# Performance work log

Measured on AMD Instinct MI355X. Metric: run time of the kernel, lower is better.

Reference implementation:

```python
import jax, jax.numpy as jnp
import numpy as np

B, S, H = 2, 2048, 1024
E, K, F = 8, 2, 4096


def setup_inputs() -> dict:
    key = jax.random.key(0)
    ks = jax.random.split(key, 7)
    s_h = 1.0 / np.sqrt(H)
    s_f = 1.0 / np.sqrt(F)
    return {
        "hidden_states": jax.random.normal(ks[0], (B, S, H), jnp.float32),
        "Wr": jax.random.normal(ks[1], (H, E), jnp.float32) * s_h,
        "br": jnp.zeros((E,), jnp.float32),
        "W1": jax.random.normal(ks[2], (E, H, F), jnp.float32) * s_h,
        "b1": jnp.zeros((E, F), jnp.float32),
        "W2": jax.random.normal(ks[3], (E, F, H), jnp.float32) * s_f,
        "b2": jnp.zeros((E, H), jnp.float32),
    }


def _moe_forward(hidden_states, Wr, br, W1, b1, W2, b2):
    b, s, h = hidden_states.shape
    x = hidden_states.reshape(-1, h)  # [T, H]
    # --- router: top-k over softmax probs, renormalized ---
    logits = x @ Wr + br  # [T, E]
    probs = jax.nn.softmax(logits, axis=-1)
    top_w, top_i = jax.lax.top_k(probs, K)  # [T, K]
    weights = top_w / jnp.sum(top_w, axis=-1, keepdims=True)  # [T, K]
    # --- dense-equivalent expert dispatch + combine ---
    # per-token per-expert combine weight (zero for unselected experts)
    out = jnp.zeros_like(x)
    for e in range(E):
        w_e = jnp.sum(weights * (top_i == e), axis=-1)  # [T]
        h_e = jax.nn.gelu(x @ W1[e] + b1[e], approximate=False)  # [T, F]
        y_e = h_e @ W2[e] + b2[e]  # [T, H]
        out = out + w_e[:, None] * y_e
    # --- aux load-balance loss (counts are constants wrt grads) ---
    counts = jnp.sum(jax.nn.one_hot(top_i, E, dtype=logits.dtype), axis=(0, 1))  # [E]
    load = counts / (top_i.size)
    aux_loss = jnp.mean((load - 1.0 / E) ** 2)
    # --- z-loss ---
    z_loss = jnp.mean(jax.nn.logsumexp(logits, axis=-1))
    total_loss = 0.01 * aux_loss + 0.001 * z_loss
    return out.reshape(b, s, h), total_loss


def reference(hidden_states, Wr, br, W1, b1, W2, b2):
    output, total_loss = _moe_forward(hidden_states, Wr, br, W1, b1, W2, b2)
    return output, total_loss
```

## Files before the change

kernel.cpp:

```cpp
#include <hip/hip_runtime.h>
#include <stdint.h>
#include <math.h>

#define T_TOK 4096
#define H_DIM 1024
#define E_EXP 8
#define F_DIM 4096
#define NASSIGN (T_TOK * 2)
#define OUT_ELEMS ((size_t)T_TOK * H_DIM)
#define YB_ELEMS ((size_t)8192 * H_DIM)
#define TL 257

typedef unsigned short u16;
typedef __attribute__((ext_vector_type(8))) short short8;
typedef __attribute__((ext_vector_type(4))) short short4v;
typedef __attribute__((ext_vector_type(4))) float f32x4;

__device__ __forceinline__ u16 f2bf(float f) {
  union { float f; uint32_t u; } c; c.f = f;
  uint32_t u = c.u;
  return (u16)((u + 0x7FFFu + ((u >> 16) & 1u)) >> 16);
}

__device__ __forceinline__ float fast_erf(float u) {
  const float au = fabsf(u);
  const float t = __builtin_amdgcn_rcpf(__builtin_fmaf(0.3275911f, au, 1.0f));
  float p = __builtin_fmaf(1.061405429f, t, -1.453152027f);
  p = __builtin_fmaf(p, t, 1.421413741f);
  p = __builtin_fmaf(p, t, -0.284496736f);
  p = __builtin_fmaf(p, t, 0.254829592f);
  p = p * t;
  const float y = __builtin_fmaf(-p, __expf(-au * au), 1.0f);
  return copysignf(y, u);
}

__device__ __forceinline__ void gl_lds16(const void* g, void* l) {
  __builtin_amdgcn_global_load_lds(
      (const __attribute__((address_space(1))) uint32_t*)g,
      (__attribute__((address_space(3))) uint32_t*)(uintptr_t)l, 16, 0, 0);
}

__device__ __forceinline__ void transpose_strip(
    const float* __restrict__ in, u16* __restrict__ out, int R, int C,
    int bx , int by , int bz, u16* tile) {
  const size_t eoff = (size_t)bz * R * C;
  const int wave = threadIdx.x >> 6, lane = threadIdx.x & 63;
  const float* inp = in + eoff + ((size_t)by * 64) * C + bx * 256;
#pragma unroll
  for (int p = 0; p < 16; ++p) {
    const int r = p * 4 + wave;
    const float4 v = *(const float4*)(inp + (size_t)r * C + lane * 4);
    u16* trow = tile + r * TL + lane * 4;
    trow[0] = f2bf(v.x); trow[1] = f2bf(v.y); trow[2] = f2bf(v.z); trow[3] = f2bf(v.w);
  }
  __syncthreads();
  const int cl = threadIdx.x >> 3;
  const int rg = (threadIdx.x & 7) * 8;
#pragma unroll
  for (int tx = 0; tx < 4; ++tx) {
    u16* op = out + (((size_t)bz * (C >> 6) + bx * 4 + tx) * (R >> 6) + by) * 4096;
#pragma unroll
    for (int p = 0; p < 2; ++p) {
      const int c = cl + p * 32;
      short8 o;
#pragma unroll
      for (int j = 0; j < 8; ++j) o[j] = (short)tile[(rg + j) * TL + tx * 64 + c];
      *(short8*)(op + c * 64 + rg) = o;
    }
  }
}

__global__ __launch_bounds__(256) void prep_kernel(
    const float* __restrict__ x, const float* __restrict__ Wr,
    const float* __restrict__ br, u16* __restrict__ xb,
    int* __restrict__ tki, float* __restrict__ tkw,
    int* __restrict__ counts, float* __restrict__ zsum,
    const float* __restrict__ W1, u16* __restrict__ w1t,
    const float* __restrict__ W2, u16* __restrict__ w2t) {
  __shared__ u16 tile[64 * TL];
  __shared__ int lcnt[8];
  __shared__ float lzv[16];
  const int id = blockIdx.x;

  if (id >= 256) {
    if (id < 2304) {
      const int q = id - 256;
      transpose_strip(W1, w1t, H_DIM, F_DIM, q & 15, (q >> 4) & 15, q >> 8, tile);
    } else {
      const int q = id - 2304;
      transpose_strip(W2, w2t, F_DIM, H_DIM, q & 3, (q >> 2) & 63, q >> 8, tile);
    }
    return;
  }

  const int wave = threadIdx.x >> 6;
  const int lane = threadIdx.x & 63;
  if (threadIdx.x < 8) lcnt[threadIdx.x] = 0;
  __syncthreads();
#pragma unroll
  for (int it = 0; it < 4; ++it) {
    const int t = id * 16 + wave * 4 + it;
    const float* xr = x + (size_t)t * H_DIM;
    u16* xbr = xb + (size_t)t * H_DIM;
    float acc[8];
#pragma unroll
    for (int e = 0; e < 8; ++e) acc[e] = 0.0f;
#pragma unroll
    for (int j = 0; j < 4; ++j) {
      const int h0 = j * 256 + lane * 4;
      const float4 xv = *(const float4*)(xr + h0);
      const float vv[4] = {xv.x, xv.y, xv.z, xv.w};
      short4v pk;
#pragma unroll
      for (int i = 0; i < 4; ++i) {
        pk[i] = (short)f2bf(vv[i]);
        const float4 w0 = *(const float4*)(Wr + (size_t)(h0 + i) * 8);
        const float4 w1 = *(const float4*)(Wr + (size_t)(h0 + i) * 8 + 4);
        acc[0] += vv[i] * w0.x; acc[1] += vv[i] * w0.y;
        acc[2] += vv[i] * w0.z; acc[3] += vv[i] * w0.w;
        acc[4] += vv[i] * w1.x; acc[5] += vv[i] * w1.y;
        acc[6] += vv[i] * w1.z; acc[7] += vv[i] * w1.w;
      }
      *(short4v*)(xbr + h0) = pk;
    }
#pragma unroll
    for (int e = 0; e < 8; ++e) {
      float v = acc[e];
#pragma unroll
      for (int s = 32; s > 0; s >>= 1) v += __shfl_xor(v, s);
      acc[e] = v;
    }
    if (lane == 0) {
      float l[8];
#pragma unroll
      for (int e = 0; e < 8; ++e) l[e] = acc[e] + br[e];
      float mx = l[0];
#pragma unroll
      for (int e = 1; e < 8; ++e) mx = fmaxf(mx, l[e]);
      float p[8], s = 0.0f;
#pragma unroll
      for (int e = 0; e < 8; ++e) { p[e] = __expf(l[e] - mx); s += p[e]; }
      int i0 = 0;
#pragma unroll
      for (int e = 1; e < 8; ++e) if (p[e] > p[i0]) i0 = e;
      int i1 = (i0 == 0) ? 1 : 0;
#pragma unroll
      for (int e = 0; e < 8; ++e) if (e != i1 && e != i0 && p[e] > p[i1]) i1 = e;
      const float ws = p[i0] + p[i1];
      tki[2 * t] = i0; tki[2 * t + 1] = i1;
      tkw[2 * t] = p[i0] / ws; tkw[2 * t + 1] = p[i1] / ws;
      atomicAdd(&lcnt[i0], 1);
      atomicAdd(&lcnt[i1], 1);
      lzv[wave * 4 + it] = mx + logf(s);
    }
  }
  __syncthreads();
  if (threadIdx.x < 8) {
    const int c = lcnt[threadIdx.x];
    if (c) atomicAdd(&counts[threadIdx.x], c);
  }
  if (threadIdx.x == 64) {
    float zs = 0.0f;
#pragma unroll
    for (int i = 0; i < 16; ++i) zs += lzv[i];
    atomicAdd(zsum, zs);
  }
}

__global__ void scatter_kernel(const int* __restrict__ tki, const float* __restrict__ tkw,
                               const int* __restrict__ counts, int* __restrict__ cursor,
                               int* __restrict__ perm, float* __restrict__ pw,
                               int* __restrict__ islot,
                               const float* __restrict__ zsum, float* __restrict__ out_loss) {
  int offs[8];
  {
    int a = 0;
#pragma unroll
    for (int e = 0; e < 8; ++e) { offs[e] = a; a += counts[e]; }
  }
  const int lane = threadIdx.x & 63;
  const int t = blockIdx.x * 256 + threadIdx.x;
#pragma unroll
  for (int k = 0; k < 2; ++k) {
    const int e = tki[2 * t + k];
    int slot = 0;
#pragma unroll
    for (int ee = 0; ee < 8; ++ee) {
      const unsigned long long mask = __ballot(e == ee);
      if (mask) {
        const int leader = __ffsll(mask) - 1;
        int b = 0;
        if (lane == leader) b = atomicAdd(&cursor[ee], (int)__popcll(mask));
        b = __shfl(b, leader);
        if (e == ee) {
          const int r = (int)__popcll(mask & ((1ull << lane) - 1ull));
          slot = offs[ee] + b + r;
        }
      }
    }
    perm[slot] = t;
    pw[slot] = tkw[2 * t + k];
    islot[2 * t + k] = slot;
  }
  if (blockIdx.x == 0 && threadIdx.x == 0) {
    float aux = 0.0f;
#pragma unroll
    for (int e = 0; e < 8; ++e) {
      const float d = (float)counts[e] / (float)NASSIGN - 0.125f;
      aux += d * d;
    }
    aux *= (1.0f / 8.0f);
    out_loss[0] = 0.01f * aux + 0.001f * (zsum[0] / (float)T_TOK);
  }
}


__global__ __launch_bounds__(256, 4) void gemm1_kernel(
    const u16* __restrict__ xb, const u16* __restrict__ w1t,
    const float* __restrict__ b1, const int* __restrict__ perm,
    const int* __restrict__ cnts, u16* __restrict__ hbuf) {
  const int id = blockIdx.x;
  const int e = id & 7;
  const int wq = id >> 3;
  const int n0 = (wq & 31) << 7;
  const int m0 = (wq >> 5) << 7;
  int cnt, off;
  {
    int a = 0, c = 0;
#pragma unroll
    for (int i = 0; i < 8; ++i) { const int ci = cnts[i]; if (i < e) a += ci; if (i == e) c = ci; }
    cnt = c; off = a;
  }
  if (m0 >= cnt) return;

  __shared__ __align__(16) u16 smem[16384];
  u16* As = smem;
  u16* Bs = smem + 8192;

  const int tid = threadIdx.x;
  const int rbase = tid >> 3;
  const int kc = ((tid & 7) ^ (rbase & 7)) * 8;

  const u16* ap[4];
#pragma unroll
  for (int l = 0; l < 4; ++l) {
    int ra = m0 + rbase + l * 32; if (ra > cnt - 1) ra = cnt - 1;
    ap[l] = xb + (size_t)perm[off + ra] * H_DIM + kc;
  }
  const u16* bp0 = w1t + ((((size_t)e * (F_DIM >> 6) + (n0 >> 6)) * (H_DIM >> 6)) << 12)
                 + rbase * 64 + kc;
  const size_t bnt = (size_t)(H_DIM >> 6) << 12;

  const int wave = tid >> 6, lane = tid & 63;
  const int wm = (wave >> 1) * 64, wn = (wave & 1) * 64;
  const int lr = lane & 15, q = lane >> 4;
  const int qs0 = q ^ (lr & 7), qs1 = (4 + q) ^ (lr & 7);

  f32x4 acc[4][4];
#pragma unroll
  for (int i = 0; i < 4; ++i)
#pragma unroll
    for (int j = 0; j < 4; ++j) acc[i][j] = (f32x4)0.0f;

  const short8* Afr = (const short8*)As;
  const short8* Bfr = (const short8*)Bs;

  for (int k0 = 0; k0 < (H_DIM >> 6); ++k0) {
    gl_lds16(ap[0], &As[(size_t)tid * 8]);
    gl_lds16(ap[1], &As[(size_t)(tid + 256) * 8]);
    gl_lds16(ap[2], &As[(size_t)(tid + 512) * 8]);
    gl_lds16(ap[3], &As[(size_t)(tid + 768) * 8]);
    gl_lds16(bp0,              &Bs[(size_t)tid * 8]);
    gl_lds16(bp0 + 2048,       &Bs[(size_t)(tid + 256) * 8]);
    gl_lds16(bp0 + bnt,        &Bs[(size_t)(tid + 512) * 8]);
    gl_lds16(bp0 + bnt + 2048, &Bs[(size_t)(tid + 768) * 8]);
#pragma unroll
    for (int l = 0; l < 4; ++l) ap[l] += 64;
    bp0 += 4096;
    __syncthreads();
#pragma unroll
    for (int s = 0; s < 2; ++s) {
      const int qs = s ? qs1 : qs0;
      short8 a[4], b[4];
#pragma unroll
      for (int i = 0; i < 4; ++i) a[i] = Afr[(wm + i * 16 + lr) * 8 + qs];
#pragma unroll
      for (int j = 0; j < 4; ++j) b[j] = Bfr[(wn + j * 16 + lr) * 8 + qs];
#pragma unroll
      for (int i = 0; i < 4; ++i)
#pragma unroll
        for (int j = 0; j < 4; ++j)
          acc[i][j] = __builtin_amdgcn_mfma_f32_16x16x32_bf16(a[i], b[j], acc[i][j], 0, 0, 0);
    }
    __syncthreads();
  }

#pragma unroll
  for (int i = 0; i < 4; ++i) {
#pragma unroll
    for (int rr = 0; rr < 4; ++rr) {
      const int row = wm + i * 16 + q * 4 + rr;
#pragma unroll
      for (int j = 0; j < 4; ++j) {
        const int col = wn + j * 16 + lr;
        const float v = acc[i][j][rr] + b1[e * F_DIM + n0 + col];
        const float g = 0.5f * v * (1.0f + fast_erf(v * 0.70710678118654752f));
        smem[(row << 7) + (col ^ (q << 4))] = f2bf(g);
      }
    }
  }
  __syncthreads();
#pragma unroll
  for (int p = 0; p < 8; ++p) {
    const int ml = p * 16 + (tid >> 4);
    const int nl = (tid & 15) * 8;
    const int m = m0 + ml;
    if (m < cnt) {
      const int qq = (ml >> 2) & 3;
      *(short8*)(hbuf + (size_t)(off + m) * F_DIM + n0 + nl) =
          *(const short8*)(smem + (ml << 7) + (nl ^ (qq << 4)));
    }
  }
}

__global__ __launch_bounds__(256, 4) void gemm2_kernel(
    const u16* __restrict__ hbuf, const u16* __restrict__ w2t,
    const float* __restrict__ b2, const float* __restrict__ pw,
    const int* __restrict__ cnts, float* __restrict__ ybuf) {
  const int id = blockIdx.x;
  const int e = id & 7;
  const int wq = id >> 3;
  const int n0 = (wq & 7) << 7;
  const int ks = (wq >> 3) & 1;
  const int m0 = (wq >> 4) << 7;
  int cnt, off;
  {
    int a = 0, c = 0;
#pragma unroll
    for (int i = 0; i < 8; ++i) { const int ci = cnts[i]; if (i < e) a += ci; if (i == e) c = ci; }
    cnt = c; off = a;
  }
  if (m0 >= cnt) return;

  __shared__ __align__(16) u16 As[128 * 64];
  __shared__ __align__(16) u16 Bs[128 * 64];

  const int tid = threadIdx.x;
  const int rbase = tid >> 3;
  const int kc = ((tid & 7) ^ (rbase & 7)) * 8;

  const u16* ap[4];
#pragma unroll
  for (int l = 0; l < 4; ++l) {
    int ra = m0 + rbase + l * 32; if (ra > cnt - 1) ra = cnt - 1;
    ap[l] = hbuf + (size_t)(off + ra) * F_DIM + (ks << 11) + kc;
  }
  const u16* bp0 = w2t + ((((size_t)e * (H_DIM >> 6) + (n0 >> 6)) * (F_DIM >> 6)) << 12)
                 + ((size_t)(ks << 5) << 12) + rbase * 64 + kc;
  const size_t bnt = (size_t)(F_DIM >> 6) << 12;

  const int wave = tid >> 6, lane = tid & 63;
  const int wm = (wave >> 1) * 64, wn = (wave & 1) * 64;
  const int lr = lane & 15, q = lane >> 4;
  const int qs0 = q ^ (lr & 7), qs1 = (4 + q) ^ (lr & 7);

  f32x4 acc[4][4];
#pragma unroll
  for (int i = 0; i < 4; ++i)
#pragma unroll
    for (int j = 0; j < 4; ++j) acc[i][j] = (f32x4)0.0f;

  const short8* Afr = (const short8*)As;
  const short8* Bfr = (const short8*)Bs;

  for (int k0 = 0; k0 < 32; ++k0) {
    gl_lds16(ap[0], &As[(size_t)tid * 8]);
    gl_lds16(ap[1], &As[(size_t)(tid + 256) * 8]);
    gl_lds16(ap[2], &As[(size_t)(tid + 512) * 8]);
    gl_lds16(ap[3], &As[(size_t)(tid + 768) * 8]);
    gl_lds16(bp0,              &Bs[(size_t)tid * 8]);
    gl_lds16(bp0 + 2048,       &Bs[(size_t)(tid + 256) * 8]);
    gl_lds16(bp0 + bnt,        &Bs[(size_t)(tid + 512) * 8]);
    gl_lds16(bp0 + bnt + 2048, &Bs[(size_t)(tid + 768) * 8]);
#pragma unroll
    for (int l = 0; l < 4; ++l) ap[l] += 64;
    bp0 += 4096;
    __syncthreads();
#pragma unroll
    for (int s = 0; s < 2; ++s) {
      const int qs = s ? qs1 : qs0;
      short8 a[4], b[4];
#pragma unroll
      for (int i = 0; i < 4; ++i) a[i] = Afr[(wm + i * 16 + lr) * 8 + qs];
#pragma unroll
      for (int j = 0; j < 4; ++j) b[j] = Bfr[(wn + j * 16 + lr) * 8 + qs];
#pragma unroll
      for (int i = 0; i < 4; ++i)
#pragma unroll
        for (int j = 0; j < 4; ++j)
          acc[i][j] = __builtin_amdgcn_mfma_f32_16x16x32_bf16(a[i], b[j], acc[i][j], 0, 0, 0);
    }
    __syncthreads();
  }

  float* yb = ybuf + (size_t)ks * YB_ELEMS;
#pragma unroll
  for (int i = 0; i < 4; ++i) {
#pragma unroll
    for (int rr = 0; rr < 4; ++rr) {
      const int m = m0 + wm + i * 16 + q * 4 + rr;
      if (m < cnt) {
        const int slot = off + m;
        const float w = pw[slot];
        float* orow = yb + (size_t)slot * H_DIM;
#pragma unroll
        for (int j = 0; j < 4; ++j) {
          const int col = n0 + wn + j * 16 + lr;
          float y = acc[i][j][rr];
          if (ks == 0) y += b2[e * H_DIM + col];
          orow[col] = w * y;
        }
      }
    }
  }
}

__global__ __launch_bounds__(256) void combine_kernel(
    const float* __restrict__ ybuf, const int* __restrict__ islot,
    float* __restrict__ out) {
  const int t = blockIdx.x;
  const int s0 = islot[2 * t];
  const int s1 = islot[2 * t + 1];
  const int c = threadIdx.x * 4;
  const float4 a0 = *(const float4*)(ybuf + (size_t)s0 * H_DIM + c);
  const float4 a1 = *(const float4*)(ybuf + YB_ELEMS + (size_t)s0 * H_DIM + c);
  const float4 b0 = *(const float4*)(ybuf + (size_t)s1 * H_DIM + c);
  const float4 b1 = *(const float4*)(ybuf + YB_ELEMS + (size_t)s1 * H_DIM + c);
  float4 r;
  r.x = a0.x + a1.x + b0.x + b1.x;
  r.y = a0.y + a1.y + b0.y + b1.y;
  r.z = a0.z + a1.z + b0.z + b1.z;
  r.w = a0.w + a1.w + b0.w + b1.w;
  *(float4*)(out + (size_t)t * H_DIM + c) = r;
}


extern "C" void kernel_launch(void* const* d_in, const int* in_sizes, int n_in,
                              void* d_out, int out_size, void* d_ws, size_t ws_size,
                              hipStream_t stream) {
  const float* x  = (const float*)d_in[0];
  const float* Wr = (const float*)d_in[1];
  const float* br = (const float*)d_in[2];
  const float* W1 = (const float*)d_in[3];
  const float* b1 = (const float*)d_in[4];
  const float* W2 = (const float*)d_in[5];
  const float* b2 = (const float*)d_in[6];
  float* out = (float*)d_out;

  char* ws = (char*)d_ws;
  u16* xb    = (u16*)(ws);
  u16* w1t   = (u16*)(ws + 8388608ull);
  u16* w2t   = (u16*)(ws + 75497472ull);
  u16* hbuf  = (u16*)(ws + 142606336ull);
  float* ybuf = (float*)(ws + 8388608ull);
  int*   tki    = (int*)(ws + 209715200ull);
  float* tkw    = (float*)(ws + 209747968ull);
  int*   perm   = (int*)(ws + 209780736ull);
  float* pw     = (float*)(ws + 209813504ull);
  int*   counts = (int*)(ws + 209846272ull);
  int*   cursor = counts + 8;
  float* zsum   = (float*)(counts + 16);
  int*   islot  = (int*)(ws + 209846400ull);

  hipMemsetAsync(counts, 0, 128, stream);

  prep_kernel<<<4352, 256, 0, stream>>>(x, Wr, br, xb, tki, tkw, counts, zsum,
                                        W1, w1t, W2, w2t);
  scatter_kernel<<<T_TOK / 256, 256, 0, stream>>>(tki, tkw, counts, cursor, perm, pw,
                                                  islot, zsum, out + OUT_ELEMS);
  gemm1_kernel<<<8192, 256, 0, stream>>>(xb, w1t, b1, perm, counts, hbuf);
  gemm2_kernel<<<4096, 256, 0, stream>>>(hbuf, w2t, b2, pw, counts, ybuf);
  combine_kernel<<<T_TOK, 256, 0, stream>>>(ybuf, islot, out);
}
```

Measured before the change: 605.9 us.

## Enlarge expert GEMM M-tile to 256 rows per block with 128x64 warp tiles

Both grouped expert GEMMs now process 256 token rows per block instead of 128, with each wave computing a 128x64 sub-tile (8x4 MFMA accumulators). This doubles reuse of each loaded weight tile and halves B-matrix global traffic per output. The GEMM1 epilogue is split into two halves so the existing shared staging buffer can still be reused. In exchange, register pressure and LDS per block rise (occupancy hint lowered to 2), and padding waste grows for experts whose token count is not a multiple of 256.

```diff
diff --git a/kernel.cpp b/kernel.cpp
--- a/kernel.cpp
+++ b/kernel.cpp
@@ -215,7 +215,7 @@
 }
 
 
-__global__ __launch_bounds__(256, 4) void gemm1_kernel(
+__global__ __launch_bounds__(256, 2) void gemm1_kernel(
     const u16* __restrict__ xb, const u16* __restrict__ w1t,
     const float* __restrict__ b1, const int* __restrict__ perm,
     const int* __restrict__ cnts, u16* __restrict__ hbuf) {
@@ -223,7 +223,7 @@
   const int e = id & 7;
   const int wq = id >> 3;
   const int n0 = (wq & 31) << 7;
-  const int m0 = (wq >> 5) << 7;
+  const int m0 = (wq >> 5) << 8;
   int cnt, off;
   {
     int a = 0, c = 0;
@@ -233,17 +233,17 @@
   }
   if (m0 >= cnt) return;
 
-  __shared__ __align__(16) u16 smem[16384];
+  __shared__ __align__(16) u16 smem[24576];
   u16* As = smem;
-  u16* Bs = smem + 8192;
+  u16* Bs = smem + 16384;
 
   const int tid = threadIdx.x;
   const int rbase = tid >> 3;
   const int kc = ((tid & 7) ^ (rbase & 7)) * 8;
 
-  const u16* ap[4];
-#pragma unroll
-  for (int l = 0; l < 4; ++l) {
+  const u16* ap[8];
+#pragma unroll
+  for (int l = 0; l < 8; ++l) {
     int ra = m0 + rbase + l * 32; if (ra > cnt - 1) ra = cnt - 1;
     ap[l] = xb + (size_t)perm[off + ra] * H_DIM + kc;
   }
@@ -252,13 +252,13 @@
   const size_t bnt = (size_t)(H_DIM >> 6) << 12;
 
   const int wave = tid >> 6, lane = tid & 63;
-  const int wm = (wave >> 1) * 64, wn = (wave & 1) * 64;
+  const int wm = (wave >> 1) * 128, wn = (wave & 1) * 64;
   const int lr = lane & 15, q = lane >> 4;
   const int qs0 = q ^ (lr & 7), qs1 = (4 + q) ^ (lr & 7);
 
-  f32x4 acc[4][4];
-#pragma unroll
-  for (int i = 0; i < 4; ++i)
+  f32x4 acc[8][4];
+#pragma unroll
+  for (int i = 0; i < 8; ++i)
 #pragma unroll
     for (int j = 0; j < 4; ++j) acc[i][j] = (f32x4)0.0f;
 
@@ -266,28 +266,27 @@
   const short8* Bfr = (const short8*)Bs;
 
   for (int k0 = 0; k0 < (H_DIM >> 6); ++k0) {
-    gl_lds16(ap[0], &As[(size_t)tid * 8]);
-    gl_lds16(ap[1], &As[(size_t)(tid + 256) * 8]);
-    gl_lds16(ap[2], &As[(size_t)(tid + 512) * 8]);
-    gl_lds16(ap[3], &As[(size_t)(tid + 768) * 8]);
+#pragma unroll
+    for (int l = 0; l < 8; ++l) {
+      gl_lds16(ap[l], &As[(size_t)(tid + l * 256) * 8]);
+      ap[l] += 64;
+    }
     gl_lds16(bp0,              &Bs[(size_t)tid * 8]);
     gl_lds16(bp0 + 2048,       &Bs[(size_t)(tid + 256) * 8]);
     gl_lds16(bp0 + bnt,        &Bs[(size_t)(tid + 512) * 8]);
     gl_lds16(bp0 + bnt + 2048, &Bs[(size_t)(tid + 768) * 8]);
-#pragma unroll
-    for (int l = 0; l < 4; ++l) ap[l] += 64;
     bp0 += 4096;
     __syncthreads();
 #pragma unroll
     for (int s = 0; s < 2; ++s) {
       const int qs = s ? qs1 : qs0;
-      short8 a[4], b[4];
-#pragma unroll
-      for (int i = 0; i < 4; ++i) a[i] = Afr[(wm + i * 16 + lr) * 8 + qs];
+      short8 a[8], b[4];
+#pragma unroll
+      for (int i = 0; i < 8; ++i) a[i] = Afr[(wm + i * 16 + lr) * 8 + qs];
 #pragma unroll
       for (int j = 0; j < 4; ++j) b[j] = Bfr[(wn + j * 16 + lr) * 8 + qs];
 #pragma unroll
-      for (int i = 0; i < 4; ++i)
+      for (int i = 0; i < 8; ++i)
 #pragma unroll
         for (int j = 0; j < 4; ++j)
           acc[i][j] = __builtin_amdgcn_mfma_f32_16x16x32_bf16(a[i], b[j], acc[i][j], 0, 0, 0);
@@ -296,34 +295,40 @@
   }
 
 #pragma unroll
-  for (int i = 0; i < 4; ++i) {
-#pragma unroll
-    for (int rr = 0; rr < 4; ++rr) {
-      const int row = wm + i * 16 + q * 4 + rr;
-#pragma unroll
-      for (int j = 0; j < 4; ++j) {
-        const int col = wn + j * 16 + lr;
-        const float v = acc[i][j][rr] + b1[e * F_DIM + n0 + col];
-        const float g = 0.5f * v * (1.0f + fast_erf(v * 0.70710678118654752f));
-        smem[(row << 7) + (col ^ (q << 4))] = f2bf(g);
+  for (int h = 0; h < 2; ++h) {
+    if ((wave >> 1) == h) {
+#pragma unroll
+      for (int i = 0; i < 8; ++i) {
+#pragma unroll
+        for (int rr = 0; rr < 4; ++rr) {
+          const int rloc = i * 16 + q * 4 + rr;
+#pragma unroll
+          for (int j = 0; j < 4; ++j) {
+            const int col = wn + j * 16 + lr;
+            const float v = acc[i][j][rr] + b1[e * F_DIM + n0 + col];
+            const float g = 0.5f * v * (1.0f + fast_erf(v * 0.70710678118654752f));
+            smem[(rloc << 7) + (col ^ (q << 4))] = f2bf(g);
+          }
+        }
       }
     }
-  }
-  __syncthreads();
-#pragma unroll
-  for (int p = 0; p < 8; ++p) {
-    const int ml = p * 16 + (tid >> 4);
-    const int nl = (tid & 15) * 8;
-    const int m = m0 + ml;
-    if (m < cnt) {
-      const int qq = (ml >> 2) & 3;
-      *(short8*)(hbuf + (size_t)(off + m) * F_DIM + n0 + nl) =
-          *(const short8*)(smem + (ml << 7) + (nl ^ (qq << 4)));
-    }
-  }
-}
-
-__global__ __launch_bounds__(256, 4) void gemm2_kernel(
+    __syncthreads();
+#pragma unroll
+    for (int p = 0; p < 8; ++p) {
+      const int ml = p * 16 + (tid >> 4);
+      const int nl = (tid & 15) * 8;
+      const int m = m0 + h * 128 + ml;
+      if (m < cnt) {
+        const int qq = (ml >> 2) & 3;
+        *(short8*)(hbuf + (size_t)(off + m) * F_DIM + n0 + nl) =
+            *(const short8*)(smem + (ml << 7) + (nl ^ (qq << 4)));
+      }
+    }
+    __syncthreads();
+  }
+}
+
+__global__ __launch_bounds__(256, 2) void gemm2_kernel(
     const u16* __restrict__ hbuf, const u16* __restrict__ w2t,
     const float* __restrict__ b2, const float* __restrict__ pw,
     const int* __restrict__ cnts, float* __restrict__ ybuf) {
@@ -332,7 +337,7 @@
   const int wq = id >> 3;
   const int n0 = (wq & 7) << 7;
   const int ks = (wq >> 3) & 1;
-  const int m0 = (wq >> 4) << 7;
+  const int m0 = (wq >> 4) << 8;
   int cnt, off;
   {
     int a = 0, c = 0;
@@ -342,16 +347,17 @@
   }
   if (m0 >= cnt) return;
 
-  __shared__ __align__(16) u16 As[128 * 64];
-  __shared__ __align__(16) u16 Bs[128 * 64];
+  __shared__ __align__(16) u16 smem[24576];
+  u16* As = smem;
+  u16* Bs = smem + 16384;
 
   const int tid = threadIdx.x;
   const int rbase = tid >> 3;
   const int kc = ((tid & 7) ^ (rbase & 7)) * 8;
 
-  const u16* ap[4];
-#pragma unroll
-  for (int l = 0; l < 4; ++l) {
+  const u16* ap[8];
+#pragma unroll
+  for (int l = 0; l < 8; ++l) {
     int ra = m0 + rbase + l * 32; if (ra > cnt - 1) ra = cnt - 1;
     ap[l] = hbuf + (size_t)(off + ra) * F_DIM + (ks << 11) + kc;
   }
@@ -360,13 +366,13 @@
   const size_t bnt = (size_t)(F_DIM >> 6) << 12;
 
   const int wave = tid >> 6, lane = tid & 63;
-  const int wm = (wave >> 1) * 64, wn = (wave & 1) * 64;
+  const int wm = (wave >> 1) * 128, wn = (wave & 1) * 64;
   const int lr = lane & 15, q = lane >> 4;
   const int qs0 = q ^ (lr & 7), qs1 = (4 + q) ^ (lr & 7);
 
-  f32x4 acc[4][4];
-#pragma unroll
-  for (int i = 0; i < 4; ++i)
+  f32x4 acc[8][4];
+#pragma unroll
+  for (int i = 0; i < 8; ++i)
 #pragma unroll
     for (int j = 0; j < 4; ++j) acc[i][j] = (f32x4)0.0f;
 
@@ -374,28 +380,27 @@
   const short8* Bfr = (const short8*)Bs;
 
   for (int k0 = 0; k0 < 32; ++k0) {
-    gl_lds16(ap[0], &As[(size_t)tid * 8]);
-    gl_lds16(ap[1], &As[(size_t)(tid + 256) * 8]);
-    gl_lds16(ap[2], &As[(size_t)(tid + 512) * 8]);
-    gl_lds16(ap[3], &As[(size_t)(tid + 768) * 8]);
+#pragma unroll
+    for (int l = 0; l < 8; ++l) {
+      gl_lds16(ap[l], &As[(size_t)(tid + l * 256) * 8]);
+      ap[l] += 64;
+    }
     gl_lds16(bp0,              &Bs[(size_t)tid * 8]);
     gl_lds16(bp0 + 2048,       &Bs[(size_t)(tid + 256) * 8]);
     gl_lds16(bp0 + bnt,        &Bs[(size_t)(tid + 512) * 8]);
     gl_lds16(bp0 + bnt + 2048, &Bs[(size_t)(tid + 768) * 8]);
-#pragma unroll
-    for (int l = 0; l < 4; ++l) ap[l] += 64;
     bp0 += 4096;
     __syncthreads();
 #pragma unroll
     for (int s = 0; s < 2; ++s) {
       const int qs = s ? qs1 : qs0;
-      short8 a[4], b[4];
-#pragma unroll
-      for (int i = 0; i < 4; ++i) a[i] = Afr[(wm + i * 16 + lr) * 8 + qs];
+      short8 a[8], b[4];
+#pragma unroll
+      for (int i = 0; i < 8; ++i) a[i] = Afr[(wm + i * 16 + lr) * 8 + qs];
 #pragma unroll
       for (int j = 0; j < 4; ++j) b[j] = Bfr[(wn + j * 16 + lr) * 8 + qs];
 #pragma unroll
-      for (int i = 0; i < 4; ++i)
+      for (int i = 0; i < 8; ++i)
 #pragma unroll
         for (int j = 0; j < 4; ++j)
           acc[i][j] = __builtin_amdgcn_mfma_f32_16x16x32_bf16(a[i], b[j], acc[i][j], 0, 0, 0);
@@ -405,7 +410,7 @@
 
   float* yb = ybuf + (size_t)ks * YB_ELEMS;
 #pragma unroll
-  for (int i = 0; i < 4; ++i) {
+  for (int i = 0; i < 8; ++i) {
 #pragma unroll
     for (int rr = 0; rr < 4; ++rr) {
       const int m = m0 + wm + i * 16 + q * 4 + rr;
@@ -478,7 +483,7 @@
                                         W1, w1t, W2, w2t);
   scatter_kernel<<<T_TOK / 256, 256, 0, stream>>>(tki, tkw, counts, cursor, perm, pw,
                                                   islot, zsum, out + OUT_ELEMS);
-  gemm1_kernel<<<8192, 256, 0, stream>>>(xb, w1t, b1, perm, counts, hbuf);
-  gemm2_kernel<<<4096, 256, 0, stream>>>(hbuf, w2t, b2, pw, counts, ybuf);
+  gemm1_kernel<<<4096, 256, 0, stream>>>(xb, w1t, b1, perm, counts, hbuf);
+  gemm2_kernel<<<2048, 256, 0, stream>>>(hbuf, w2t, b2, pw, counts, ybuf);
   combine_kernel<<<T_TOK, 256, 0, stream>>>(ybuf, islot, out);
 }
```

New measurement: 586.2 us. 3.2% less time.

## Double-buffer GEMM A tiles, load B into registers, overlap W2 transpose with gemm1

Applied to the files above, without the earlier changes.

Both expert GEMMs now stage A tiles into two alternating LDS buffers and read B fragments directly from global memory into registers. Explicit vmcnt waits and raw barriers replace the per-iteration full syncthreads, so the next tile's loads overlap the current tile's MFMAs. The W2 transpose moves out of the prep kernel and into extra blocks of the gemm1 launch, so it can run alongside gemm1 instead of on the prep critical path. In exchange, register pressure rises (launch bounds drop to 3 blocks/CU), and the larger shared buffer in gemm1 lowers occupancy.

```diff
diff --git a/kernel.cpp b/kernel.cpp
--- a/kernel.cpp
+++ b/kernel.cpp
@@ -75,21 +75,15 @@
     const float* __restrict__ br, u16* __restrict__ xb,
     int* __restrict__ tki, float* __restrict__ tkw,
     int* __restrict__ counts, float* __restrict__ zsum,
-    const float* __restrict__ W1, u16* __restrict__ w1t,
-    const float* __restrict__ W2, u16* __restrict__ w2t) {
+    const float* __restrict__ W1, u16* __restrict__ w1t) {
   __shared__ u16 tile[64 * TL];
   __shared__ int lcnt[8];
   __shared__ float lzv[16];
   const int id = blockIdx.x;
 
   if (id >= 256) {
-    if (id < 2304) {
-      const int q = id - 256;
-      transpose_strip(W1, w1t, H_DIM, F_DIM, q & 15, (q >> 4) & 15, q >> 8, tile);
-    } else {
-      const int q = id - 2304;
-      transpose_strip(W2, w2t, F_DIM, H_DIM, q & 3, (q >> 2) & 63, q >> 8, tile);
-    }
+    const int q = id - 256;
+    transpose_strip(W1, w1t, H_DIM, F_DIM, q & 15, (q >> 4) & 15, q >> 8, tile);
     return;
   }
 
@@ -215,11 +209,59 @@
 }
 
 
-__global__ __launch_bounds__(256, 4) void gemm1_kernel(
+#define STAGEA(NB)                                                        \
+  { _Pragma("unroll")                                                     \
+    for (int l = 0; l < 4; ++l) {                                         \
+      gl_lds16(ap[l], &smem[(NB) + ((size_t)tid + l * 256) * 8]);         \
+      ap[l] += 64;                                                        \
+    } }
+
+#define LOADB(DST)                                                        \
+  { _Pragma("unroll")                                                     \
+    for (int j = 0; j < 4; ++j) {                                         \
+      _Pragma("unroll")                                                   \
+      for (int s = 0; s < 2; ++s)                                         \
+        DST[j][s] = bgp[(j * 16 + lr) * 8 + s * 4 + q];                   \
+    }                                                                     \
+    bgp += 512; }
+
+#define COMPUTE(NB, BC)                                                   \
+  { const short8* Afr = (const short8*)(smem + (NB));                     \
+    _Pragma("unroll")                                                     \
+    for (int s = 0; s < 2; ++s) {                                         \
+      const int qs = s ? qs1 : qs0;                                       \
+      short8 a[4];                                                        \
+      _Pragma("unroll")                                                   \
+      for (int i = 0; i < 4; ++i) a[i] = Afr[(wm + i * 16 + lr) * 8 + qs];\
+      _Pragma("unroll")                                                   \
+      for (int i = 0; i < 4; ++i)                                         \
+        _Pragma("unroll")                                                 \
+        for (int j = 0; j < 4; ++j)                                       \
+          acc[i][j] = __builtin_amdgcn_mfma_f32_16x16x32_bf16(            \
+              a[i], BC[j][s], acc[i][j], 0, 0, 0);                        \
+    } }
+
+#define VWAIT12 asm volatile("s_waitcnt vmcnt(12)" ::: "memory");         \
+                __builtin_amdgcn_sched_barrier(0);                        \
+                __builtin_amdgcn_s_barrier();
+#define VWAIT0  asm volatile("s_waitcnt vmcnt(0)" ::: "memory");          \
+                __builtin_amdgcn_sched_barrier(0);                        \
+                __builtin_amdgcn_s_barrier();
+
+__global__ __launch_bounds__(256, 3) void gemm1_kernel(
     const u16* __restrict__ xb, const u16* __restrict__ w1t,
     const float* __restrict__ b1, const int* __restrict__ perm,
-    const int* __restrict__ cnts, u16* __restrict__ hbuf) {
+    const int* __restrict__ cnts, u16* __restrict__ hbuf,
+    const float* __restrict__ W2, u16* __restrict__ w2t) {
+  __shared__ __align__(16) u16 smem[64 * TL];
   const int id = blockIdx.x;
+
+  if (id >= 8192) {
+    const int q = id - 8192;
+    transpose_strip(W2, w2t, F_DIM, H_DIM, q & 3, (q >> 2) & 63, q >> 8, smem);
+    return;
+  }
+
   const int e = id & 7;
   const int wq = id >> 3;
   const int n0 = (wq & 31) << 7;
@@ -233,10 +275,6 @@
   }
   if (m0 >= cnt) return;
 
-  __shared__ __align__(16) u16 smem[16384];
-  u16* As = smem;
-  u16* Bs = smem + 8192;
-
   const int tid = threadIdx.x;
   const int rbase = tid >> 3;
   const int kc = ((tid & 7) ^ (rbase & 7)) * 8;
@@ -247,54 +285,41 @@
     int ra = m0 + rbase + l * 32; if (ra > cnt - 1) ra = cnt - 1;
     ap[l] = xb + (size_t)perm[off + ra] * H_DIM + kc;
   }
-  const u16* bp0 = w1t + ((((size_t)e * (F_DIM >> 6) + (n0 >> 6)) * (H_DIM >> 6)) << 12)
-                 + rbase * 64 + kc;
-  const size_t bnt = (size_t)(H_DIM >> 6) << 12;
 
   const int wave = tid >> 6, lane = tid & 63;
-  const int wm = (wave >> 1) * 64, wn = (wave & 1) * 64;
+  const int wm = (wave >> 1) * 64;
   const int lr = lane & 15, q = lane >> 4;
   const int qs0 = q ^ (lr & 7), qs1 = (4 + q) ^ (lr & 7);
 
+  const int nt = (n0 >> 6) + (wave & 1);
+  const short8* bgp = (const short8*)(w1t +
+      ((((size_t)e * (F_DIM >> 6) + nt) * (H_DIM >> 6)) << 12));
+
   f32x4 acc[4][4];
 #pragma unroll
   for (int i = 0; i < 4; ++i)
 #pragma unroll
     for (int j = 0; j < 4; ++j) acc[i][j] = (f32x4)0.0f;
 
-  const short8* Afr = (const short8*)As;
-  const short8* Bfr = (const short8*)Bs;
-
-  for (int k0 = 0; k0 < (H_DIM >> 6); ++k0) {
-    gl_lds16(ap[0], &As[(size_t)tid * 8]);
-    gl_lds16(ap[1], &As[(size_t)(tid + 256) * 8]);
-    gl_lds16(ap[2], &As[(size_t)(tid + 512) * 8]);
-    gl_lds16(ap[3], &As[(size_t)(tid + 768) * 8]);
-    gl_lds16(bp0,              &Bs[(size_t)tid * 8]);
-    gl_lds16(bp0 + 2048,       &Bs[(size_t)(tid + 256) * 8]);
-    gl_lds16(bp0 + bnt,        &Bs[(size_t)(tid + 512) * 8]);
-    gl_lds16(bp0 + bnt + 2048, &Bs[(size_t)(tid + 768) * 8]);
-#pragma unroll
-    for (int l = 0; l < 4; ++l) ap[l] += 64;
-    bp0 += 4096;
-    __syncthreads();
-#pragma unroll
-    for (int s = 0; s < 2; ++s) {
-      const int qs = s ? qs1 : qs0;
-      short8 a[4], b[4];
-#pragma unroll
-      for (int i = 0; i < 4; ++i) a[i] = Afr[(wm + i * 16 + lr) * 8 + qs];
-#pragma unroll
-      for (int j = 0; j < 4; ++j) b[j] = Bfr[(wn + j * 16 + lr) * 8 + qs];
-#pragma unroll
-      for (int i = 0; i < 4; ++i)
-#pragma unroll
-        for (int j = 0; j < 4; ++j)
-          acc[i][j] = __builtin_amdgcn_mfma_f32_16x16x32_bf16(a[i], b[j], acc[i][j], 0, 0, 0);
-    }
-    __syncthreads();
-  }
-
+  short8 bA[4][2], bB[4][2];
+  STAGEA(0); LOADB(bA);
+
+  for (int k0 = 0; k0 < (H_DIM >> 6); k0 += 2) {
+    STAGEA(8192); LOADB(bB);
+    VWAIT12;
+    COMPUTE(0, bA);
+    __builtin_amdgcn_s_barrier();
+    if (k0 + 2 < (H_DIM >> 6)) {
+      STAGEA(0); LOADB(bA);
+      VWAIT12;
+    } else {
+      VWAIT0;
+    }
+    COMPUTE(8192, bB);
+    __builtin_amdgcn_s_barrier();
+  }
+
+  const int wn = (wave & 1) * 64;
 #pragma unroll
   for (int i = 0; i < 4; ++i) {
 #pragma unroll
@@ -323,10 +348,11 @@
   }
 }
 
-__global__ __launch_bounds__(256, 4) void gemm2_kernel(
+__global__ __launch_bounds__(256, 3) void gemm2_kernel(
     const u16* __restrict__ hbuf, const u16* __restrict__ w2t,
     const float* __restrict__ b2, const float* __restrict__ pw,
     const int* __restrict__ cnts, float* __restrict__ ybuf) {
+  __shared__ __align__(16) u16 smem[16384];
   const int id = blockIdx.x;
   const int e = id & 7;
   const int wq = id >> 3;
@@ -342,9 +368,6 @@
   }
   if (m0 >= cnt) return;
 
-  __shared__ __align__(16) u16 As[128 * 64];
-  __shared__ __align__(16) u16 Bs[128 * 64];
-
   const int tid = threadIdx.x;
   const int rbase = tid >> 3;
   const int kc = ((tid & 7) ^ (rbase & 7)) * 8;
@@ -355,54 +378,41 @@
     int ra = m0 + rbase + l * 32; if (ra > cnt - 1) ra = cnt - 1;
     ap[l] = hbuf + (size_t)(off + ra) * F_DIM + (ks << 11) + kc;
   }
-  const u16* bp0 = w2t + ((((size_t)e * (H_DIM >> 6) + (n0 >> 6)) * (F_DIM >> 6)) << 12)
-                 + ((size_t)(ks << 5) << 12) + rbase * 64 + kc;
-  const size_t bnt = (size_t)(F_DIM >> 6) << 12;
 
   const int wave = tid >> 6, lane = tid & 63;
-  const int wm = (wave >> 1) * 64, wn = (wave & 1) * 64;
+  const int wm = (wave >> 1) * 64;
   const int lr = lane & 15, q = lane >> 4;
   const int qs0 = q ^ (lr & 7), qs1 = (4 + q) ^ (lr & 7);
 
+  const int nt = (n0 >> 6) + (wave & 1);
+  const short8* bgp = (const short8*)(w2t +
+      (((size_t)e * (H_DIM >> 6) + nt) * (F_DIM >> 6) + (ks << 5)) * 4096);
+
   f32x4 acc[4][4];
 #pragma unroll
   for (int i = 0; i < 4; ++i)
 #pragma unroll
     for (int j = 0; j < 4; ++j) acc[i][j] = (f32x4)0.0f;
 
-  const short8* Afr = (const short8*)As;
-  const short8* Bfr = (const short8*)Bs;
-
-  for (int k0 = 0; k0 < 32; ++k0) {
-    gl_lds16(ap[0], &As[(size_t)tid * 8]);
-    gl_lds16(ap[1], &As[(size_t)(tid + 256) * 8]);
-    gl_lds16(ap[2], &As[(size_t)(tid + 512) * 8]);
-    gl_lds16(ap[3], &As[(size_t)(tid + 768) * 8]);
-    gl_lds16(bp0,              &Bs[(size_t)tid * 8]);
-    gl_lds16(bp0 + 2048,       &Bs[(size_t)(tid + 256) * 8]);
-    gl_lds16(bp0 + bnt,        &Bs[(size_t)(tid + 512) * 8]);
-    gl_lds16(bp0 + bnt + 2048, &Bs[(size_t)(tid + 768) * 8]);
-#pragma unroll
-    for (int l = 0; l < 4; ++l) ap[l] += 64;
-    bp0 += 4096;
-    __syncthreads();
-#pragma unroll
-    for (int s = 0; s < 2; ++s) {
-      const int qs = s ? qs1 : qs0;
-      short8 a[4], b[4];
-#pragma unroll
-      for (int i = 0; i < 4; ++i) a[i] = Afr[(wm + i * 16 + lr) * 8 + qs];
-#pragma unroll
-      for (int j = 0; j < 4; ++j) b[j] = Bfr[(wn + j * 16 + lr) * 8 + qs];
-#pragma unroll
-      for (int i = 0; i < 4; ++i)
-#pragma unroll
-        for (int j = 0; j < 4; ++j)
-          acc[i][j] = __builtin_amdgcn_mfma_f32_16x16x32_bf16(a[i], b[j], acc[i][j], 0, 0, 0);
-    }
-    __syncthreads();
-  }
-
+  short8 bA[4][2], bB[4][2];
+  STAGEA(0); LOADB(bA);
+
+  for (int k0 = 0; k0 < 32; k0 += 2) {
+    STAGEA(8192); LOADB(bB);
+    VWAIT12;
+    COMPUTE(0, bA);
+    __builtin_amdgcn_s_barrier();
+    if (k0 + 2 < 32) {
+      STAGEA(0); LOADB(bA);
+      VWAIT12;
+    } else {
+      VWAIT0;
+    }
+    COMPUTE(8192, bB);
+    __builtin_amdgcn_s_barrier();
+  }
+
+  const int wn = (wave & 1) * 64;
   float* yb = ybuf + (size_t)ks * YB_ELEMS;
 #pragma unroll
   for (int i = 0; i < 4; ++i) {
@@ -474,11 +484,10 @@
 
   hipMemsetAsync(counts, 0, 128, stream);
 
-  prep_kernel<<<4352, 256, 0, stream>>>(x, Wr, br, xb, tki, tkw, counts, zsum,
-                                        W1, w1t, W2, w2t);
+  prep_kernel<<<2304, 256, 0, stream>>>(x, Wr, br, xb, tki, tkw, counts, zsum, W1, w1t);
   scatter_kernel<<<T_TOK / 256, 256, 0, stream>>>(tki, tkw, counts, cursor, perm, pw,
                                                   islot, zsum, out + OUT_ELEMS);
-  gemm1_kernel<<<8192, 256, 0, stream>>>(xb, w1t, b1, perm, counts, hbuf);
+  gemm1_kernel<<<10240, 256, 0, stream>>>(xb, w1t, b1, perm, counts, hbuf, W2, w2t);
   gemm2_kernel<<<4096, 256, 0, stream>>>(hbuf, w2t, b2, pw, counts, ybuf);
   combine_kernel<<<T_TOK, 256, 0, stream>>>(ybuf, islot, out);
 }
```

Measured after the change: 1.089 ms. 1.8x slower.
